# Performance work log

Measured on AMD Instinct MI355X. Metric: run time of the kernel, lower is better.

The kernel has to match this reference:

```python
import jax, jax.numpy as jnp
import numpy as np

N = 100000
E = 1600000
IN_C, HID_C, OUT_C = 128, 64, 64
LAYERS = 2


def setup_inputs() -> dict:
    key = jax.random.key(0)
    ks = jax.random.split(key, 7)
    x = jax.random.normal(ks[0], (N, IN_C), dtype=jnp.float32)
    edge_index = jax.random.randint(ks[1], (2, E), 0, N, dtype=jnp.int32)
    W_init = jax.random.normal(ks[2], (IN_C, HID_C), dtype=jnp.float32) / np.sqrt(IN_C)
    W_self = jax.random.normal(ks[3], (LAYERS, HID_C, HID_C), dtype=jnp.float32) / np.sqrt(HID_C)
    W_agg = jax.random.normal(ks[4], (LAYERS, HID_C, HID_C), dtype=jnp.float32) / np.sqrt(HID_C)
    b = jnp.zeros((LAYERS, HID_C), dtype=jnp.float32)
    W_out = jax.random.normal(ks[5], (HID_C, OUT_C), dtype=jnp.float32) / np.sqrt(HID_C)
    return {"x": x, "edge_index": edge_index, "W_init": W_init,
            "W_self": W_self, "W_agg": W_agg, "b": b, "W_out": W_out}


def reference(x, edge_index, W_init, W_self, W_agg, b, W_out):
    # edge (dst, src): aggregated_neighbors[edge[0]].append(x[edge[1]])
    dst = edge_index[0]
    src = edge_index[1]
    n = x.shape[0]
    # in-degree for mean aggregation (clamp to 1 for isolated nodes)
    deg = jax.ops.segment_sum(jnp.ones((src.shape[0],), dtype=x.dtype), dst,
                              num_segments=n)
    deg = jnp.maximum(deg, 1.0)[:, None]  # [N,1]
    h = x @ W_init  # initialize: [N, hid]
    for l in range(LAYERS):
        msgs = h[src]  # per-edge gather [E, hid]
        agg = jax.ops.segment_sum(msgs, dst, num_segments=n) / deg  # mean aggregate
        h = jax.nn.relu(agg @ W_agg[l] + h @ W_self[l] + b[l])  # combine
    return h @ W_out  # output: [N, out]
```

## Files before the change

kernel.cpp:

```cpp
#include <hip/hip_runtime.h>
#include <hip/hip_fp16.h>

#define N_NODES 100000
#define E_EDGES 1600000
#define IN_C    128
#define HID_C   64
#define OUT_C   64
#define ROWS    32
#define NBUCK   391
#define BSHIFT  8
#define BNODES  256
#define CAP     5120
#define CHUNK   4096
#define NB_BINCH 391
#define NB_TR   112
#define IDXCAP  1632
#define IDXMAX  1568

typedef _Float16 f16x8 __attribute__((ext_vector_type(8)));
typedef float    f32x4 __attribute__((ext_vector_type(4)));
#define MFMA16(a, b, c) __builtin_amdgcn_mfma_f32_16x16x32_f16(a, b, c, 0, 0, 0)

struct BinS {
    int hist[NBUCK]; int resbase[NBUCK]; int cur[NBUCK];
    unsigned pk[CHUNK]; unsigned short bk[CHUNK];
};

__global__ __launch_bounds__(256) void k1_bin_tr(const int* __restrict__ ei,
                                                 int* __restrict__ bucket_cursor,
                                                 unsigned* __restrict__ gbuck,
                                                 const float* __restrict__ Wi,
                                                 const float* __restrict__ Wsf,
                                                 const float* __restrict__ Waf,
                                                 const float* __restrict__ Wo,
                                                 _Float16* __restrict__ wtr) {
    __shared__ BinS S;
    int tid = threadIdx.x;
    if (blockIdx.x < NB_BINCH) {
        for (int i = tid; i < NBUCK; i += 256) S.hist[i] = 0;
        __syncthreads();
        int base = blockIdx.x * CHUNK;
        for (int i = tid; i < CHUNK; i += 256) {
            int e = base + i;
            if (e < E_EDGES) {
                int dst = ei[e];
                int src = ei[E_EDGES + e];
                int b = dst >> BSHIFT;
                S.pk[i] = ((unsigned)(dst & (BNODES - 1)) << 17) | (unsigned)src;
                S.bk[i] = (unsigned short)b;
                atomicAdd(&S.hist[b], 1);
            } else S.bk[i] = 0xFFFF;
        }
        __syncthreads();
        for (int i = tid; i < NBUCK; i += 256) {
            S.resbase[i] = atomicAdd(&bucket_cursor[i], S.hist[i]);
            S.cur[i] = 0;
        }
        __syncthreads();
        for (int i = tid; i < CHUNK; i += 256) {
            if (S.bk[i] != 0xFFFF) {
                int b = S.bk[i];
                int slot = S.resbase[b] + atomicAdd(&S.cur[b], 1);
                if (slot < CAP) gbuck[(size_t)b * CAP + slot] = S.pk[i];
            }
        }
    } else {
        int t = (blockIdx.x - NB_BINCH) * 256 + tid;
        if (t < 8192) {
            int k = t >> 6, col = t & 63;
            wtr[col * 136 + k] = (_Float16)Wi[t];
        } else if (t < 24576) {
            int u = t - 8192; int l = u >> 13; int v = u & 8191;
            int k = v >> 6, col = v & 63;
            float w = (k < 64) ? Waf[l * 4096 + k * 64 + col] : Wsf[l * 4096 + (k - 64) * 64 + col];
            wtr[8704 + l * 8704 + col * 136 + k] = (_Float16)w;
        } else if (t < 28672) {
            int u = t - 24576; int k = u >> 6, col = u & 63;
            wtr[26112 + col * 72 + k] = (_Float16)Wo[u];
        }
    }
}

struct InitS { _Float16 sA[ROWS][IN_C + 8]; _Float16 sBt[HID_C][IN_C + 8]; };
struct BuildS { int lcnt[BNODES]; int lpos[BNODES]; int lcur[BNODES]; int s[2][512]; };
union K2S { InitS ini; BuildS bld; };

template<int K>
__device__ __forceinline__ void mfma_tile(const _Float16* sA, const _Float16* sBt,
                                          int lane, int wave, f32x4 acc[2]) {
    const int LDA = K + 8;
    int r0 = (wave >> 1) * 16;
    int wc = wave & 1;
    int m = lane & 15, kg = lane >> 4;
    acc[0] = (f32x4){0.f, 0.f, 0.f, 0.f};
    acc[1] = (f32x4){0.f, 0.f, 0.f, 0.f};
    #pragma unroll
    for (int ks = 0; ks < K / 32; ++ks) {
        f16x8 a = *(const f16x8*)&sA[(r0 + m) * LDA + 32 * ks + 8 * kg];
        #pragma unroll
        for (int nt = 0; nt < 2; ++nt) {
            f16x8 b = *(const f16x8*)&sBt[(wc * 32 + nt * 16 + m) * LDA + 32 * ks + 8 * kg];
            acc[nt] = MFMA16(a, b, acc[nt]);
        }
    }
}

template<int NKS>
__device__ __forceinline__ void mfma_regB(const _Float16* aBase, int lda, int m,
                                          int kg, const f16x8* bf0, const f16x8* bf1,
                                          f32x4 acc[2]) {
    #pragma unroll
    for (int ks = 0; ks < NKS; ++ks) {
        f16x8 a = *(const f16x8*)&aBase[m * lda + 32 * ks + 8 * kg];
        acc[0] = MFMA16(a, bf0[ks], acc[0]);
        acc[1] = MFMA16(a, bf1[ks], acc[1]);
    }
}

__global__ __launch_bounds__(256) void k2_build_init(const unsigned* __restrict__ gbuck,
                                                     const int* __restrict__ bucket_cursor,
                                                     int* __restrict__ csr,
                                                     int2* __restrict__ rc,
                                                     const float* __restrict__ x,
                                                     const float4* __restrict__ wtrI,
                                                     __half* __restrict__ h) {
    __shared__ K2S U;
    int t = threadIdx.x;
    if (blockIdx.x < NBUCK) {
        BuildS& S = U.bld;
        int b = blockIdx.x;
        int v0 = (t < NBUCK) ? min(bucket_cursor[t], CAP) : 0;
        int v1 = (t + 256 < NBUCK) ? min(bucket_cursor[t + 256], CAP) : 0;
        S.s[0][t] = v0; S.s[0][t + 256] = v1;
        S.lcnt[t] = 0; S.lcur[t] = 0;
        __syncthreads();
        int p = 0;
        for (int off = 1; off < 512; off <<= 1) {
            int a0 = S.s[p][t]       + ((t >= off)       ? S.s[p][t - off] : 0);
            int a1 = S.s[p][t + 256] + ((t + 256 >= off) ? S.s[p][t + 256 - off] : 0);
            S.s[p ^ 1][t] = a0; S.s[p ^ 1][t + 256] = a1;
            __syncthreads();
            p ^= 1;
        }
        int bb = (b == 0) ? 0 : S.s[p][b - 1];
        int ec = min(bucket_cursor[b], CAP);
        int gnode = b * BNODES;
        int nn = min(BNODES, N_NODES - gnode);
        const unsigned* mybuck = gbuck + (size_t)b * CAP;
        __syncthreads();
        for (int i = t; i < ec; i += 256) atomicAdd(&S.lcnt[mybuck[i] >> 17], 1);
        __syncthreads();
        int c = S.lcnt[t];
        S.s[0][t] = c;
        __syncthreads();
        int q = 0;
        for (int off = 1; off < 256; off <<= 1) {
            int a0 = S.s[q][t] + ((t >= off) ? S.s[q][t - off] : 0);
            S.s[q ^ 1][t] = a0;
            __syncthreads();
            q ^= 1;
        }
        int ex = S.s[q][t] - c;
        S.lpos[t] = ex;
        if (t < nn) rc[gnode + t] = make_int2(bb + ex, c);
        __syncthreads();
        for (int i = t; i < ec; i += 256) {
            unsigned pkt = mybuck[i];
            int dl = pkt >> 17;
            int slot = S.lpos[dl] + atomicAdd(&S.lcur[dl], 1);
            csr[bb + slot] = (int)(pkt & 0x1FFFF);
        }
    } else {
        InitS& S = U.ini;
        int row0 = (blockIdx.x - NBUCK) * ROWS;
        float4* sB4 = (float4*)&S.sBt[0][0];
        for (int i = t; i < 1088; i += 256) sB4[i] = wtrI[i];
        const float4* x4 = (const float4*)x;
        for (int i = t; i < ROWS * 32; i += 256) {
            int r = i >> 5, qq = i & 31;
            float4 f = x4[(size_t)(row0 + r) * 32 + qq];
            __half2 ha = __floats2half2_rn(f.x, f.y), hb = __floats2half2_rn(f.z, f.w);
            uint2 u; u.x = *(unsigned*)&ha; u.y = *(unsigned*)&hb;
            *(uint2*)&S.sA[r][qq * 4] = u;
        }
        __syncthreads();
        int lane = t & 63, wave = t >> 6;
        f32x4 acc[2];
        mfma_tile<IN_C>(&S.sA[0][0], &S.sBt[0][0], lane, wave, acc);
        int m = lane & 15, rg = lane >> 4;
        int r0 = (wave >> 1) * 16, wc = wave & 1;
        #pragma unroll
        for (int nt = 0; nt < 2; ++nt) {
            int col = wc * 32 + nt * 16 + m;
            #pragma unroll
            for (int i = 0; i < 4; ++i) {
                int row = row0 + r0 + rg * 4 + i;
                h[(size_t)row * HID_C + col] = __float2half(acc[nt][i]);
            }
        }
    }
}

template<bool FINAL>
__global__ __launch_bounds__(256, 5) void fused_layer(const __half* __restrict__ h,
                                                      const int2* __restrict__ rc,
                                                      const int* __restrict__ csr,
                                                      const _Float16* __restrict__ wB,
                                                      const float* __restrict__ bias,
                                                      __half* __restrict__ hout,
                                                      const _Float16* __restrict__ wO,
                                                      float* __restrict__ out) {
    __shared__ _Float16 sA[ROWS][136];
    __shared__ int sIdx[IDXCAP];
    __shared__ int2 sRC[ROWS];
    int tid = threadIdx.x;
    int wave = tid >> 6, lane = tid & 63;
    int m = lane & 15, kg = lane >> 4, wc = wave & 1;
    int row0 = blockIdx.x * ROWS;
    const uint2* h2u = (const uint2*)h;

    f16x8 bf0[4], bf1[4];
    #pragma unroll
    for (int ks = 0; ks < 4; ++ks) {
        bf0[ks] = *(const f16x8*)&wB[(wc * 32 + m) * 136 + 32 * ks + 8 * kg];
        bf1[ks] = *(const f16x8*)&wB[(wc * 32 + 16 + m) * 136 + 32 * ks + 8 * kg];
    }

    if (tid < 32) sRC[tid] = rc[row0 + tid];
    int2 rcF = rc[row0];
    int2 rcL = rc[row0 + 31];
    int e0 = __builtin_amdgcn_readfirstlane(rcF.x);
    int e1 = __builtin_amdgcn_readfirstlane(rcL.x) + __builtin_amdgcn_readfirstlane(rcL.y);
    int Lc = min(e1 - e0, IDXMAX);
    for (int i = tid; i < Lc; i += 256) sIdx[i] = csr[e0 + i];
    if (tid < 64) sIdx[min(Lc + tid, IDXCAP - 1)] = 0;
    for (int i = tid; i < 512; i += 256) {
        int r = i >> 4, qq = i & 15;
        *(uint2*)&sA[r][64 + qq * 4] = h2u[(size_t)(row0 + r) * 16 + qq];
    }
    __syncthreads();

    int g4 = lane >> 4;
    int c16 = lane & 15;
    int sl[8], dd[8];
    int dmax = 0;
    #pragma unroll
    for (int r = 0; r < 8; ++r) {
        int2 v = sRC[wave * 8 + r];
        sl[r] = min(__builtin_amdgcn_readfirstlane(v.x) - e0, IDXMAX);
        dd[r] = __builtin_amdgcn_readfirstlane(v.y);
        dmax = max(dmax, dd[r]);
    }
    const __half2 hzero = __floats2half2_rn(0.f, 0.f);
    __half2 p01[8], p23[8];
    #pragma unroll
    for (int r = 0; r < 8; ++r) { p01[r] = hzero; p23[r] = hzero; }

    for (int c8 = 0; c8 < dmax; c8 += 8) {
        #pragma unroll
        for (int r = 0; r < 8; ++r) {
            if (c8 < dd[r]) {
                #pragma unroll
                for (int s = 0; s < 2; ++s) {
                    int ee = c8 + s * 4 + g4;
                    int src = sIdx[sl[r] + ee];
                    uint2 vv = h2u[(size_t)src * 16 + c16];
                    bool ok = ee < dd[r];
                    unsigned vx = ok ? vv.x : 0u, vy = ok ? vv.y : 0u;
                    p01[r] += *(__half2*)&vx;
                    p23[r] += *(__half2*)&vy;
                }
            }
        }
    }

    #pragma unroll
    for (int r = 0; r < 8; ++r) {
        unsigned u01 = *(unsigned*)&p01[r], u23 = *(unsigned*)&p23[r];
        unsigned o01 = (unsigned)__shfl_xor((int)u01, 16);
        unsigned o23 = (unsigned)__shfl_xor((int)u23, 16);
        p01[r] += *(__half2*)&o01; p23[r] += *(__half2*)&o23;
        u01 = *(unsigned*)&p01[r]; u23 = *(unsigned*)&p23[r];
        o01 = (unsigned)__shfl_xor((int)u01, 32);
        o23 = (unsigned)__shfl_xor((int)u23, 32);
        p01[r] += *(__half2*)&o01; p23[r] += *(__half2*)&o23;
        if (lane < 16) {
            __half2 hinv = __float2half2_rn(1.f / fmaxf((float)dd[r], 1.f));
            __half2 q01 = p01[r] * hinv, q23 = p23[r] * hinv;
            uint2 agg2; agg2.x = *(unsigned*)&q01; agg2.y = *(unsigned*)&q23;
            *(uint2*)&sA[wave * 8 + r][4 * c16] = agg2;
        }
    }
    __syncthreads();

    f32x4 acc[2];
    acc[0] = (f32x4){0.f, 0.f, 0.f, 0.f};
    acc[1] = (f32x4){0.f, 0.f, 0.f, 0.f};
    int r0 = (wave >> 1) * 16;
    mfma_regB<4>(&sA[r0][0], 136, m, kg, bf0, bf1, acc);
    int rg = lane >> 4;
    if (!FINAL) {
        #pragma unroll
        for (int nt = 0; nt < 2; ++nt) {
            int col = wc * 32 + nt * 16 + m;
            float bv = bias[col];
            f32x4 a = (nt == 0) ? acc[0] : acc[1];
            #pragma unroll
            for (int i = 0; i < 4; ++i) {
                int row = row0 + r0 + rg * 4 + i;
                hout[(size_t)row * HID_C + col] = __float2half(fmaxf(a[i] + bv, 0.f));
            }
        }
    } else {
        __syncthreads();
        _Float16* sA72 = &sA[0][0];
        #pragma unroll
        for (int nt = 0; nt < 2; ++nt) {
            int col = wc * 32 + nt * 16 + m;
            float bv = bias[col];
            f32x4 a = (nt == 0) ? acc[0] : acc[1];
            #pragma unroll
            for (int i = 0; i < 4; ++i) {
                int rl = r0 + rg * 4 + i;
                sA72[rl * 72 + col] = (_Float16)fmaxf(a[i] + bv, 0.f);
            }
        }
        f16x8 of0[2], of1[2];
        #pragma unroll
        for (int ks = 0; ks < 2; ++ks) {
            of0[ks] = *(const f16x8*)&wO[(wc * 32 + m) * 72 + 32 * ks + 8 * kg];
            of1[ks] = *(const f16x8*)&wO[(wc * 32 + 16 + m) * 72 + 32 * ks + 8 * kg];
        }
        __syncthreads();
        f32x4 acc2[2];
        acc2[0] = (f32x4){0.f, 0.f, 0.f, 0.f};
        acc2[1] = (f32x4){0.f, 0.f, 0.f, 0.f};
        mfma_regB<2>(&sA72[r0 * 72], 72, m, kg, of0, of1, acc2);
        #pragma unroll
        for (int nt = 0; nt < 2; ++nt) {
            int col = wc * 32 + nt * 16 + m;
            f32x4 a = (nt == 0) ? acc2[0] : acc2[1];
            #pragma unroll
            for (int i = 0; i < 4; ++i) {
                int row = row0 + r0 + rg * 4 + i;
                out[(size_t)row * OUT_C + col] = a[i];
            }
        }
    }
}

extern "C" void kernel_launch(void* const* d_in, const int* in_sizes, int n_in,
                              void* d_out, int out_size, void* d_ws, size_t ws_size,
                              hipStream_t stream) {
    const float* x      = (const float*)d_in[0];
    const int*   ei     = (const int*)  d_in[1];
    const float* W_init = (const float*)d_in[2];
    const float* W_self = (const float*)d_in[3];
    const float* W_agg  = (const float*)d_in[4];
    const float* b      = (const float*)d_in[5];
    const float* W_out  = (const float*)d_in[6];
    float* out = (float*)d_out;

    char* ws = (char*)d_ws;
    const size_t KB = 1 << 10;
    int*      bucket_cursor = (int*)(ws + 0);
    int2*     rc            = (int2*)(ws + 4 * KB);
    int*      csr           = (int*)(ws + 1024 * KB);
    _Float16* wtr           = (_Float16*)(ws + 7424 * KB);
    unsigned* gbuck         = (unsigned*)(ws + 8192 * KB);
    __half*   hA            = (__half*)(ws + 18432 * KB);
    __half*   hB            = (__half*)(ws + 32768 * KB);

    const float4*   wtrI  = (const float4*)(wtr);
    const _Float16* wtrL0 = wtr + 8704;
    const _Float16* wtrL1 = wtr + 17408;
    const _Float16* wtrO  = wtr + 26112;

    hipMemsetAsync(bucket_cursor, 0, NBUCK * sizeof(int), stream);
    k1_bin_tr<<<NB_BINCH + NB_TR, 256, 0, stream>>>(ei, bucket_cursor, gbuck,
                                                    W_init, W_self, W_agg, W_out, wtr);
    k2_build_init<<<NBUCK + N_NODES / ROWS, 256, 0, stream>>>(gbuck, bucket_cursor, csr, rc,
                                                              x, wtrI, hA);
    const int GB = N_NODES / ROWS;
    fused_layer<false><<<GB, 256, 0, stream>>>(hA, rc, csr, wtrL0, b + 0 * HID_C, hB,
                                               wtrO, out);
    fused_layer<true><<<GB, 256, 0, stream>>>(hB, rc, csr, wtrL1, b + 1 * HID_C, hA,
                                              wtrO, out);
}
```

Before: 136.9 us.

## Widen neighbor gathers to 16-byte loads and defer weight register loads

The gather loop now loads each 64-channel fp16 row as eight 16-byte chunks, so 8 edges are in flight per wave instead of 4 edges with 8-byte chunks, and the reduction uses one more shuffle stage. The MFMA weight fragments are loaded after aggregation rather than before, which shortens their register live range and supports raising the launch-bounds occupancy hint from 5 to 8 blocks. The aim is fewer, wider memory transactions and more resident waves to hide gather latency. The cost is more shuffles, and the higher occupancy target may force register spills.

After: 142.6 us. +4.2%, slower.

```diff
diff --git a/kernel.cpp b/kernel.cpp
--- a/kernel.cpp
+++ b/kernel.cpp
@@ -202,7 +202,7 @@
 }
 
 template<bool FINAL>
-__global__ __launch_bounds__(256, 5) void fused_layer(const __half* __restrict__ h,
+__global__ __launch_bounds__(256, 8) void fused_layer(const __half* __restrict__ h,
                                                       const int2* __restrict__ rc,
                                                       const int* __restrict__ csr,
                                                       const _Float16* __restrict__ wB,
@@ -217,14 +217,7 @@
     int wave = tid >> 6, lane = tid & 63;
     int m = lane & 15, kg = lane >> 4, wc = wave & 1;
     int row0 = blockIdx.x * ROWS;
-    const uint2* h2u = (const uint2*)h;
-
-    f16x8 bf0[4], bf1[4];
-    #pragma unroll
-    for (int ks = 0; ks < 4; ++ks) {
-        bf0[ks] = *(const f16x8*)&wB[(wc * 32 + m) * 136 + 32 * ks + 8 * kg];
-        bf1[ks] = *(const f16x8*)&wB[(wc * 32 + 16 + m) * 136 + 32 * ks + 8 * kg];
-    }
+    const uint4* h4 = (const uint4*)h;
 
     if (tid < 32) sRC[tid] = rc[row0 + tid];
     int2 rcF = rc[row0];
@@ -234,14 +227,14 @@
     int Lc = min(e1 - e0, IDXMAX);
     for (int i = tid; i < Lc; i += 256) sIdx[i] = csr[e0 + i];
     if (tid < 64) sIdx[min(Lc + tid, IDXCAP - 1)] = 0;
-    for (int i = tid; i < 512; i += 256) {
-        int r = i >> 4, qq = i & 15;
-        *(uint2*)&sA[r][64 + qq * 4] = h2u[(size_t)(row0 + r) * 16 + qq];
+    {
+        int r = tid >> 3, qq = tid & 7;
+        *(uint4*)&sA[r][64 + qq * 8] = h4[(size_t)(row0 + r) * 8 + qq];
     }
     __syncthreads();
 
-    int g4 = lane >> 4;
-    int c16 = lane & 15;
+    int e8  = lane >> 3;
+    int c8l = lane & 7;
     int sl[8], dd[8];
     int dmax = 0;
     #pragma unroll
@@ -252,44 +245,61 @@
         dmax = max(dmax, dd[r]);
     }
     const __half2 hzero = __floats2half2_rn(0.f, 0.f);
-    __half2 p01[8], p23[8];
-    #pragma unroll
-    for (int r = 0; r < 8; ++r) { p01[r] = hzero; p23[r] = hzero; }
+    __half2 p[8][4];
+    #pragma unroll
+    for (int r = 0; r < 8; ++r) {
+        #pragma unroll
+        for (int tctr = 0; tctr < 4; ++tctr) p[r][tctr] = hzero;
+    }
 
     for (int c8 = 0; c8 < dmax; c8 += 8) {
         #pragma unroll
         for (int r = 0; r < 8; ++r) {
             if (c8 < dd[r]) {
-                #pragma unroll
-                for (int s = 0; s < 2; ++s) {
-                    int ee = c8 + s * 4 + g4;
-                    int src = sIdx[sl[r] + ee];
-                    uint2 vv = h2u[(size_t)src * 16 + c16];
-                    bool ok = ee < dd[r];
-                    unsigned vx = ok ? vv.x : 0u, vy = ok ? vv.y : 0u;
-                    p01[r] += *(__half2*)&vx;
-                    p23[r] += *(__half2*)&vy;
-                }
+                int ee = c8 + e8;
+                int src = sIdx[sl[r] + ee];
+                uint4 vv = h4[(size_t)src * 8 + c8l];
+                bool ok = ee < dd[r];
+                unsigned w0 = ok ? vv.x : 0u, w1 = ok ? vv.y : 0u;
+                unsigned w2 = ok ? vv.z : 0u, w3 = ok ? vv.w : 0u;
+                p[r][0] += *(__half2*)&w0;
+                p[r][1] += *(__half2*)&w1;
+                p[r][2] += *(__half2*)&w2;
+                p[r][3] += *(__half2*)&w3;
             }
         }
     }
 
     #pragma unroll
     for (int r = 0; r < 8; ++r) {
-        unsigned u01 = *(unsigned*)&p01[r], u23 = *(unsigned*)&p23[r];
-        unsigned o01 = (unsigned)__shfl_xor((int)u01, 16);
-        unsigned o23 = (unsigned)__shfl_xor((int)u23, 16);
-        p01[r] += *(__half2*)&o01; p23[r] += *(__half2*)&o23;
-        u01 = *(unsigned*)&p01[r]; u23 = *(unsigned*)&p23[r];
-        o01 = (unsigned)__shfl_xor((int)u01, 32);
-        o23 = (unsigned)__shfl_xor((int)u23, 32);
-        p01[r] += *(__half2*)&o01; p23[r] += *(__half2*)&o23;
-        if (lane < 16) {
+        #pragma unroll
+        for (int tctr = 0; tctr < 4; ++tctr) {
+            unsigned u = *(unsigned*)&p[r][tctr];
+            unsigned o8  = (unsigned)__shfl_xor((int)u, 8);
+            p[r][tctr] += *(__half2*)&o8;
+            u = *(unsigned*)&p[r][tctr];
+            unsigned o16 = (unsigned)__shfl_xor((int)u, 16);
+            p[r][tctr] += *(__half2*)&o16;
+            u = *(unsigned*)&p[r][tctr];
+            unsigned o32 = (unsigned)__shfl_xor((int)u, 32);
+            p[r][tctr] += *(__half2*)&o32;
+        }
+        if (lane < 8) {
             __half2 hinv = __float2half2_rn(1.f / fmaxf((float)dd[r], 1.f));
-            __half2 q01 = p01[r] * hinv, q23 = p23[r] * hinv;
-            uint2 agg2; agg2.x = *(unsigned*)&q01; agg2.y = *(unsigned*)&q23;
-            *(uint2*)&sA[wave * 8 + r][4 * c16] = agg2;
-        }
+            __half2 q0 = p[r][0] * hinv, q1 = p[r][1] * hinv;
+            __half2 q2 = p[r][2] * hinv, q3 = p[r][3] * hinv;
+            uint4 o;
+            o.x = *(unsigned*)&q0; o.y = *(unsigned*)&q1;
+            o.z = *(unsigned*)&q2; o.w = *(unsigned*)&q3;
+            *(uint4*)&sA[wave * 8 + r][8 * lane] = o;
+        }
+    }
+
+    f16x8 bf0[4], bf1[4];
+    #pragma unroll
+    for (int ks = 0; ks < 4; ++ks) {
+        bf0[ks] = *(const f16x8*)&wB[(wc * 32 + m) * 136 + 32 * ks + 8 * kg];
+        bf1[ks] = *(const f16x8*)&wB[(wc * 32 + 16 + m) * 136 + 32 * ks + 8 * kg];
     }
     __syncthreads();
 
```
